# Kernel optimization log

Measured on AMD Instinct MI355X. Metric: run time of the kernel, lower is better.

The kernel has to match this reference:

```python
import jax, jax.numpy as jnp
import numpy as np

N_NODES = 100000
N_QUERIES = 128
D = 128
E = 131072

def leaky(x):
    return jax.nn.leaky_relu(x, negative_slope=0.01)

def setup_inputs() -> dict:
    key = jax.random.key(0)
    ks = jax.random.split(key, 16)
    inp = {
        'visited_node_score': jax.random.uniform(ks[0], (N_NODES,), jnp.float32),
        'node_rep': jax.random.normal(ks[1], (N_NODES, D), jnp.float32),
        'query_src_ts_emb': jax.random.normal(ks[2], (N_QUERIES, D), jnp.float32),
        'query_rel_emb': jax.random.normal(ks[3], (N_QUERIES, D), jnp.float32),
        'rel_emb': jax.random.normal(ks[4], (E, D), jnp.float32),
        'W_left': jax.random.normal(ks[5], (2 * D, 4 * D), jnp.float32) * np.sqrt(2.0 / (4 * D)),
        'b_left': jnp.zeros((2 * D,), jnp.float32),
        'W_right': jax.random.normal(ks[6], (2 * D, 4 * D), jnp.float32) * np.sqrt(2.0 / (4 * D)),
        'b_right': jnp.zeros((2 * D,), jnp.float32),
        'W_center': jax.random.normal(ks[7], (2 * D, 2 * D), jnp.float32) * np.sqrt(2.0 / (4 * D)),
        'b_center': jnp.zeros((2 * D,), jnp.float32),
        'W_step': jax.random.normal(ks[8], (D, D), jnp.float32) * np.sqrt(2.0 / (2 * D)),
        'b_step': jnp.zeros((D,), jnp.float32),
        'query_idx': jax.random.randint(ks[9], (E,), 0, N_QUERIES, jnp.int32),
        'idx_i': jax.random.randint(ks[10], (E,), 0, N_NODES, jnp.int32),
        'idx_j': jax.random.randint(ks[11], (E,), 0, N_NODES, jnp.int32),
        'max_edges': 1024,
    }
    return inp

def _forward(visited_node_score, node_rep, query_src_ts_emb, query_rel_emb, rel_emb,
             W_left, b_left, W_right, b_right, W_center, b_center, W_step, b_step,
             query_idx, idx_i, idx_j, max_edges):
    num_nodes = node_rep.shape[0]
    num_q = query_src_ts_emb.shape[0]
    e = rel_emb.shape[0]
    # gathers (irregular access)
    hi = node_rep[idx_i]            # [E, D]
    hj = node_rep[idx_j]            # [E, D]
    qs = query_src_ts_emb[query_idx]  # [E, D]
    qr = query_rel_emb[query_idx]     # [E, D]
    # G bilinear module: sum(leaky(L x) * C(leaky(R y)), -1)
    left_x = jnp.concatenate([hi, rel_emb, qs, qr], axis=-1)   # [E, 4D]
    right_x = jnp.concatenate([hj, rel_emb, qs, qr], axis=-1)  # [E, 4D]
    l = leaky(left_x @ W_left.T + b_left)                      # [E, 2D]
    r = leaky(right_x @ W_right.T + b_right) @ W_center.T + b_center  # [E, 2D]
    logits = jnp.sum(l * r, axis=-1)                           # [E]
    # segment softmax over source node idx (idx_i), as segment_softmax_op_v2
    seg_max = jax.ops.segment_max(logits, idx_i, num_segments=num_nodes)
    ex = jnp.exp(logits - seg_max[idx_i])
    denom = jax.ops.segment_sum(ex, idx_i, num_segments=num_nodes)
    attn = ex / denom[idx_i]                                   # [E]
    src_score = visited_node_score[idx_i]
    target_score = attn * src_score                            # [E]
    # per-query-group top-k pruning (mask instead of dynamic-shape slice)
    order = jnp.lexsort((-target_score, query_idx))            # sort by group, score desc
    g_sorted = query_idx[order]
    pos = jnp.arange(e, dtype=jnp.int32)
    starts = jax.ops.segment_min(pos, g_sorted, num_segments=num_q)
    rank_sorted = pos - starts[g_sorted]
    rank = jnp.zeros((e,), jnp.int32).at[order].set(rank_sorted)
    keep = (rank < max_edges).astype(logits.dtype)             # [E]
    # sum aggregation of pruned target scores into target nodes (sparse mm)
    updated_node_score = jax.ops.segment_sum(keep * target_score, idx_j, num_segments=num_nodes)
    # update node representation along pruned edges (attention-weighted message passing)
    attn_pruned = keep * attn
    agg = jax.ops.segment_sum(attn_pruned[:, None] * hi, idx_j, num_segments=num_nodes)
    new_rep = node_rep + agg
    # bypass_forward: linear_between_steps + LeakyReLU
    out_rep = leaky(new_rep @ W_step.T + b_step)
    return updated_node_score, out_rep

def reference(visited_node_score, node_rep, query_src_ts_emb, query_rel_emb, rel_emb,
              W_left, b_left, W_right, b_right, W_center, b_center, W_step, b_step,
              query_idx, idx_i, idx_j, max_edges):
    return _forward(visited_node_score, node_rep, query_src_ts_emb, query_rel_emb, rel_emb,
                    W_left, b_left, W_right, b_right, W_center, b_center, W_step, b_step,
                    query_idx, idx_i, idx_j, max_edges)
```

## Files before the change

### kernel.cpp

```cpp
#include <hip/hip_runtime.h>

typedef unsigned short u16;
typedef unsigned int   u32;
typedef __attribute__((ext_vector_type(8))) short short8;
typedef __attribute__((ext_vector_type(4))) short short4v;
typedef __attribute__((ext_vector_type(4))) float f32x4;

#define N_NODES 100000
#define NQ      128
#define DD      128
#define NE      131072
#define OO      256

__device__ __forceinline__ float b2f(u16 b){ u32 u = ((u32)b) << 16; return __uint_as_float(u); }
__device__ __forceinline__ u16 f2b(float f){ u32 u = __float_as_uint(f); u32 r = (u + 0x7FFFu + ((u >> 16) & 1u)) >> 16; return (u16)r; }
__device__ __forceinline__ float lrelu(float x){ return x > 0.0f ? x : 0.01f * x; }
__device__ __forceinline__ u32 fenc(float f){ u32 u = __float_as_uint(f); return (u & 0x80000000u) ? ~u : (u | 0x80000000u); }
__device__ __forceinline__ float fdec(u32 e){ u32 u = (e & 0x80000000u) ? (e & 0x7FFFFFFFu) : ~e; return __uint_as_float(u); }

__device__ __forceinline__ void stage4(f32x4 v, u16* dhi, u16* dlo){
  short4v h4, l4;
  #pragma unroll
  for (int i = 0; i < 4; ++i){
    u16 h = f2b(v[i]); h4[i] = (short)h; l4[i] = (short)f2b(v[i] - b2f(h));
  }
  *(short4v*)dhi = h4; *(short4v*)dlo = l4;
}

__device__ __forceinline__ void cvt4(f32x4 v, short4v& h4, short4v& l4){
  #pragma unroll
  for (int i = 0; i < 4; ++i){
    u16 h = f2b(v[i]); h4[i] = (short)h; l4[i] = (short)f2b(v[i] - b2f(h));
  }
}

#define SPL_N1 (256*512)
#define SPL_N2 (256*512)
#define SPL_N3 (256*256)
#define SPL_N4 (128*128)
__global__ void split_all_kernel(
    const float* __restrict__ Wl, const float* __restrict__ Wr,
    const float* __restrict__ Wc, const float* __restrict__ Ws,
    u16* __restrict__ WlH, u16* __restrict__ WlL,
    u16* __restrict__ WrH, u16* __restrict__ WrL,
    u16* __restrict__ WcH, u16* __restrict__ WcL,
    u16* __restrict__ WsH, u16* __restrict__ WsL)
{
  int i = blockIdx.x*256 + threadIdx.x;
  const float* src; u16 *hi, *lo; int k = i;
  if (k < SPL_N1){ src = Wl; hi = WlH; lo = WlL; }
  else if ((k -= SPL_N1) < SPL_N2){ src = Wr; hi = WrH; lo = WrL; }
  else if ((k -= SPL_N2) < SPL_N3){ src = Wc; hi = WcH; lo = WcL; }
  else if ((k -= SPL_N3) < SPL_N4){ src = Ws; hi = WsH; lo = WsL; }
  else return;
  float x = src[k];
  u16 h = f2b(x);
  hi[k] = h;
  lo[k] = f2b(x - b2f(h));
}

__global__ __launch_bounds__(256) void qtable_kernel(
    const float* __restrict__ qsrc, const float* __restrict__ qrel,
    const float* __restrict__ Wl, const float* __restrict__ bl,
    const float* __restrict__ Wr, const float* __restrict__ br,
    float* __restrict__ Qlt, float* __restrict__ Qrt)
{
  int b = blockIdx.x; int side = b >> 7; int q = b & 127; int o = threadIdx.x;
  __shared__ __align__(16) float s[2*DD];
  __shared__ float sW[256*17];
  if (o < DD) s[o] = qsrc[q*DD + o];
  else        s[o] = qrel[q*DD + o - DD];
  const float* W    = side ? Wr : Wl;
  const float* bias = side ? br : bl;
  float acc = bias[o];
  for (int kt = 0; kt < 16; ++kt){
    __syncthreads();
    for (int f = o; f < 4096; f += 256){
      int oo = f >> 4, kk = f & 15;
      sW[oo*17 + kk] = W[(size_t)oo*512 + 256 + kt*16 + kk];
    }
    __syncthreads();
    #pragma unroll
    for (int kk = 0; kk < 16; ++kk)
      acc += s[kt*16 + kk] * sW[o*17 + kk];
  }
  (side ? Qrt : Qlt)[q*OO + o] = acc;
}

#define BM   64
#define RSTc 264
#define HST  136

template<int WS>
__device__ __forceinline__ void gemm8(f32x4 (&ACC)[4][2],
    const u16* __restrict__ WH, const u16* __restrict__ WL,
    const u16* A0H, const u16* A0L, const u16* A1H, const u16* A1L, int ASTR,
    int ow, int ln, int qd)
{
  short8 pbh[2][2], pbl[2][2];
  #pragma unroll
  for (int d = 0; d < 2; ++d)
    #pragma unroll
    for (int nt = 0; nt < 2; ++nt){ int o = ow + nt*16 + ln;
      pbh[d][nt] = *(const short8*)(WH + (size_t)o*WS + d*32 + qd*8);
      pbl[d][nt] = *(const short8*)(WL + (size_t)o*WS + d*32 + qd*8);
    }
  #pragma unroll
  for (int c = 0; c < 8; ++c){
    const u16* hs = (c < 4) ? A0H : A1H;
    const u16* ls = (c < 4) ? A0L : A1L;
    int cc = (c < 4) ? c : c - 4;
    short8 bh[2], bl[2];
    #pragma unroll
    for (int nt = 0; nt < 2; ++nt){ bh[nt] = pbh[c&1][nt]; bl[nt] = pbl[c&1][nt]; }
    if (c < 6){
      #pragma unroll
      for (int nt = 0; nt < 2; ++nt){ int o = ow + nt*16 + ln;
        pbh[c&1][nt] = *(const short8*)(WH + (size_t)o*WS + (c+2)*32 + qd*8);
        pbl[c&1][nt] = *(const short8*)(WL + (size_t)o*WS + (c+2)*32 + qd*8);
      }
    }
    #pragma unroll
    for (int mp = 0; mp < 2; ++mp){
      short8 ah[2], al[2];
      #pragma unroll
      for (int k = 0; k < 2; ++k){
        int base = ((mp*2 + k)*16 + ln)*ASTR + cc*32 + qd*8;
        ah[k] = *(const short8*)&hs[base];
        al[k] = *(const short8*)&ls[base];
      }
      #pragma unroll
      for (int k = 0; k < 2; ++k)
        #pragma unroll
        for (int nt = 0; nt < 2; ++nt)
          ACC[mp*2+k][nt] = __builtin_amdgcn_mfma_f32_16x16x32_bf16(ah[k], bh[nt], ACC[mp*2+k][nt], 0, 0, 0);
      #pragma unroll
      for (int k = 0; k < 2; ++k)
        #pragma unroll
        for (int nt = 0; nt < 2; ++nt)
          ACC[mp*2+k][nt] = __builtin_amdgcn_mfma_f32_16x16x32_bf16(ah[k], bl[nt], ACC[mp*2+k][nt], 0, 0, 0);
      #pragma unroll
      for (int k = 0; k < 2; ++k)
        #pragma unroll
        for (int nt = 0; nt < 2; ++nt)
          ACC[mp*2+k][nt] = __builtin_amdgcn_mfma_f32_16x16x32_bf16(al[k], bh[nt], ACC[mp*2+k][nt], 0, 0, 0);
    }
  }
}

__global__ __launch_bounds__(512, 4) void edge_logits_kernel(
    const float* __restrict__ node_rep, const float* __restrict__ rel_emb,
    const u16* __restrict__ WlH, const u16* __restrict__ WlL,
    const u16* __restrict__ WrH, const u16* __restrict__ WrL,
    const u16* __restrict__ WcH, const u16* __restrict__ WcL,
    const float* __restrict__ bcb,
    const float* __restrict__ Qlt, const float* __restrict__ Qrt,
    const int* __restrict__ idx_i, const int* __restrict__ idx_j, const int* __restrict__ qidx,
    float* __restrict__ logits, u32* __restrict__ segmax, int* __restrict__ qcount)
{
  __shared__ __align__(16) u16 bufA[2*BM*HST];
  __shared__ __align__(16) u16 bufB[2*BM*HST];
  __shared__ int qidS[BM];
  __shared__ float lpart[8][BM];

  u16* HjHi = bufA;  u16* HjLo = bufA + BM*HST;
  u16* ReHi = bufB;  u16* ReLo = bufB + BM*HST;
  u16* RRhi = bufA;  u16* RRlo = bufB;

  const int tid = threadIdx.x;
  const int e0 = blockIdx.x * BM;
  const int lane = tid & 63, w = tid >> 6;
  const int ln = lane & 15, qd = lane >> 4;
  const int ow = w * 32;

  if (tid < BM) qidS[tid] = qidx[e0 + tid];

  #pragma unroll
  for (int it = 0; it < 4; ++it){
    int c = tid + it*512;
    int r = c >> 5, seg = (c & 31) << 2;
    int j = idx_j[e0 + r];
    f32x4 vj = *(const f32x4*)(node_rep + (size_t)j*DD + seg);
    f32x4 vr = *(const f32x4*)(rel_emb + (size_t)(e0 + r)*DD + seg);
    stage4(vj, &HjHi[r*HST + seg], &HjLo[r*HST + seg]);
    stage4(vr, &ReHi[r*HST + seg], &ReLo[r*HST + seg]);
  }
  short4v hpreH[4], hpreL[4];
  #pragma unroll
  for (int it = 0; it < 4; ++it){
    int c = tid + it*512;
    int r = c >> 5, seg = (c & 31) << 2;
    f32x4 v = *(const f32x4*)(node_rep + (size_t)idx_i[e0 + r]*DD + seg);
    cvt4(v, hpreH[it], hpreL[it]);
  }
  __syncthreads();

  f32x4 acc[4][2];
  #pragma unroll
  for (int mt = 0; mt < 4; ++mt)
    #pragma unroll
    for (int nt = 0; nt < 2; ++nt) acc[mt][nt] = (f32x4){0.f,0.f,0.f,0.f};
  gemm8<512>(acc, WrH, WrL, HjHi, HjLo, ReHi, ReLo, HST, ow, ln, qd);
  __syncthreads();

  #pragma unroll
  for (int it = 0; it < 4; ++it){
    int c = tid + it*512;
    int r = c >> 5, seg = (c & 31) << 2;
    *(short4v*)&HjHi[r*HST + seg] = hpreH[it];
    *(short4v*)&HjLo[r*HST + seg] = hpreL[it];
  }
  __syncthreads();

  f32x4 lacc[4][2];
  #pragma unroll
  for (int mt = 0; mt < 4; ++mt)
    #pragma unroll
    for (int nt = 0; nt < 2; ++nt) lacc[mt][nt] = (f32x4){0.f,0.f,0.f,0.f};
  gemm8<512>(lacc, WlH, WlL, HjHi, HjLo, ReHi, ReLo, HST, ow, ln, qd);
  __syncthreads();

  #pragma unroll
  for (int mt = 0; mt < 4; ++mt)
    #pragma unroll
    for (int nt = 0; nt < 2; ++nt){
      int col = ow + nt*16 + ln;
      #pragma unroll
      for (int rg = 0; rg < 4; ++rg){
        int row = mt*16 + qd*4 + rg;
        float v = acc[mt][nt][rg] + Qrt[qidS[row]*OO + col];
        v = lrelu(v);
        u16 hi = f2b(v);
        RRhi[row*RSTc + col] = hi;
        RRlo[row*RSTc + col] = f2b(v - b2f(hi));
      }
    }
  __syncthreads();

  f32x4 racc[4][2];
  #pragma unroll
  for (int mt = 0; mt < 4; ++mt)
    #pragma unroll
    for (int nt = 0; nt < 2; ++nt) racc[mt][nt] = (f32x4){0.f,0.f,0.f,0.f};
  gemm8<256>(racc, WcH, WcL, RRhi, RRlo, RRhi + 128, RRlo + 128, RSTc, ow, ln, qd);

  float bcv[2];
  #pragma unroll
  for (int nt = 0; nt < 2; ++nt) bcv[nt] = bcb[ow + nt*16 + ln];

  float part[4][4];
  #pragma unroll
  for (int mt = 0; mt < 4; ++mt)
    #pragma unroll
    for (int rg = 0; rg < 4; ++rg) part[mt][rg] = 0.f;

  #pragma unroll
  for (int mt = 0; mt < 4; ++mt)
    #pragma unroll
    for (int nt = 0; nt < 2; ++nt){
      int col = ow + nt*16 + ln;
      #pragma unroll
      for (int rg = 0; rg < 4; ++rg){
        int row = mt*16 + qd*4 + rg;
        float lv = lacc[mt][nt][rg] + Qlt[qidS[row]*OO + col];
        lv = lrelu(lv);
        float rv = racc[mt][nt][rg] + bcv[nt];
        part[mt][rg] += lv * rv;
      }
    }

  #pragma unroll
  for (int mt = 0; mt < 4; ++mt)
    #pragma unroll
    for (int rg = 0; rg < 4; ++rg){
      float p = part[mt][rg];
      p += __shfl_xor(p, 1); p += __shfl_xor(p, 2);
      p += __shfl_xor(p, 4); p += __shfl_xor(p, 8);
      if (ln == 0) lpart[w][mt*16 + qd*4 + rg] = p;
    }
  __syncthreads();
  if (tid < BM){
    float lg = lpart[0][tid] + lpart[1][tid] + lpart[2][tid] + lpart[3][tid]
             + lpart[4][tid] + lpart[5][tid] + lpart[6][tid] + lpart[7][tid];
    int e = e0 + tid;
    logits[e] = lg;
    atomicMax(segmax + idx_i[e], fenc(lg));
    atomicAdd(qcount + qidx[e], 1);
  }
}

__global__ void seg_exp_sum_kernel(const float* __restrict__ logits,
    const int* __restrict__ idx_i, const u32* __restrict__ segmax,
    float* __restrict__ ex, float* __restrict__ denom)
{
  int e = blockIdx.x*256 + threadIdx.x; if (e >= NE) return;
  int i = idx_i[e];
  float d = fminf(logits[e] - fdec(segmax[i]), 0.0f);
  float v = expf(d);
  ex[e] = v;
  atomicAdd(denom + i, v);
}

__global__ __launch_bounds__(128) void scan_kernel(const int* __restrict__ qcount,
                            int* __restrict__ qstart, int* __restrict__ qcursor)
{
  __shared__ int s[NQ];
  int t = threadIdx.x;
  int mine = qcount[t];
  s[t] = mine;
  __syncthreads();
  #pragma unroll
  for (int off = 1; off < NQ; off <<= 1){
    int v = (t >= off) ? s[t - off] : 0;
    __syncthreads();
    s[t] += v;
    __syncthreads();
  }
  int excl = s[t] - mine;
  qstart[t] = excl;
  qcursor[t] = excl;
}

__global__ void attn_bucket_kernel(const float* __restrict__ ex,
    const float* __restrict__ denom, const int* __restrict__ idx_i,
    const float* __restrict__ visited, const int* __restrict__ qidx,
    int* __restrict__ qcursor, int* __restrict__ bucket,
    float* __restrict__ attn, float* __restrict__ target)
{
  int e = blockIdx.x*256 + threadIdx.x; if (e >= NE) return;
  int i = idx_i[e];
  float a = ex[e] / fmaxf(denom[i], 1e-30f);
  attn[e] = a;
  target[e] = a * visited[i];
  int p = atomicAdd(qcursor + qidx[e], 1);
  bucket[p] = e;
}

#define TOPK_CAP 2560
__global__ __launch_bounds__(1024) void topk_kernel(
    const int* __restrict__ qcount, const int* __restrict__ qstart,
    const int* __restrict__ bucket, const float* __restrict__ target,
    const int* __restrict__ maxe_p, int* __restrict__ keep)
{
  __shared__ float ss[TOPK_CAP];
  __shared__ int   se[TOPK_CAP];
  int q = blockIdx.x;
  int m = qcount[q], start = qstart[q];
  int maxe = *maxe_p;
  if (maxe <= 0 || maxe > (1 << 30)){
    float f = __int_as_float(maxe);
    if (f > 0.0f && f < 1.0e9f) maxe = (int)f;
  }
  int tid = threadIdx.x;
  if (m <= maxe){
    for (int i = tid; i < m; i += 1024) keep[bucket[start + i]] = 1;
    return;
  }
  if (m <= TOPK_CAP){
    for (int i = tid; i < m; i += 1024){
      int e = bucket[start + i]; ss[i] = target[e]; se[i] = e;
    }
    __syncthreads();
    for (int i = tid; i < m; i += 1024){
      float s = ss[i]; int eid = se[i]; int cnt = 0;
      for (int j = 0; j < m; ++j){
        float sj = ss[j]; int ej = se[j];
        cnt += (sj > s) || (sj == s && ej < eid);
      }
      keep[eid] = (cnt < maxe) ? 1 : 0;
    }
  } else {
    for (int i = tid; i < m; i += 1024){
      int eid = bucket[start + i]; float s = target[eid]; int cnt = 0;
      for (int j = 0; j < m; ++j){
        int ej = bucket[start + j]; float sj = target[ej];
        cnt += (sj > s) || (sj == s && ej < eid);
      }
      keep[eid] = (cnt < maxe) ? 1 : 0;
    }
  }
}

__global__ __launch_bounds__(256) void edge_scatter_kernel(
    const int* __restrict__ keep, const float* __restrict__ attn,
    const float* __restrict__ target,
    const int* __restrict__ idx_i, const int* __restrict__ idx_j,
    const float* __restrict__ node_rep,
    float* __restrict__ out_score, float* __restrict__ agg)
{
  int wid = (blockIdx.x * 256 + threadIdx.x) >> 6;
  if (wid >= NE) return;
  if (!keep[wid]) return;
  int lane = threadIdx.x & 63;
  int ii = idx_i[wid], jj = idx_j[wid];
  float a = attn[wid];
  if (lane == 0) atomicAdd(out_score + jj, target[wid]);
  float h0 = node_rep[(size_t)ii*DD + lane];
  float h1 = node_rep[(size_t)ii*DD + 64 + lane];
  atomicAdd(agg + (size_t)jj*DD + lane,      a*h0);
  atomicAdd(agg + (size_t)jj*DD + 64 + lane, a*h1);
}

__global__ __launch_bounds__(256) void final_mfma_kernel(
    const float* __restrict__ node_rep, const float* __restrict__ aggc,
    const u16* __restrict__ WsH, const u16* __restrict__ WsL,
    const float* __restrict__ bstep, float* __restrict__ out_rep)
{
  __shared__ __align__(16) u16 Ahi[64*HST];
  __shared__ __align__(16) u16 Alo[64*HST];
  const int tid = threadIdx.x;
  const int m0 = blockIdx.x * 64;

  for (int c = tid; c < 64*32; c += 256){
    int r = c >> 5, seg = (c & 31) << 2;
    int m = m0 + r;
    float v[4];
    if (m < N_NODES){
      const float* nr = node_rep + (size_t)m*DD + seg;
      const float* ag = aggc + (size_t)m*DD + seg;
      #pragma unroll
      for (int i = 0; i < 4; ++i) v[i] = nr[i] + ag[i];
    } else {
      #pragma unroll
      for (int i = 0; i < 4; ++i) v[i] = 0.f;
    }
    short4v h4, l4;
    #pragma unroll
    for (int i = 0; i < 4; ++i){
      u16 h = f2b(v[i]); h4[i] = (short)h; l4[i] = (short)f2b(v[i] - b2f(h));
    }
    *(short4v*)&Ahi[r*HST + seg] = h4;
    *(short4v*)&Alo[r*HST + seg] = l4;
  }
  __syncthreads();

  const int lane = tid & 63, w = tid >> 6;
  const int ln = lane & 15, qd = lane >> 4;
  const int ow = w * 32;

  short8 bh[2][4], bl[2][4];
  #pragma unroll
  for (int nt = 0; nt < 2; ++nt)
    #pragma unroll
    for (int c = 0; c < 4; ++c){
      int o = ow + nt*16 + ln;
      bh[nt][c] = *(const short8*)(WsH + (size_t)o*DD + c*32 + qd*8);
      bl[nt][c] = *(const short8*)(WsL + (size_t)o*DD + c*32 + qd*8);
    }

  f32x4 acc[4][2];
  #pragma unroll
  for (int mt = 0; mt < 4; ++mt)
    #pragma unroll
    for (int nt = 0; nt < 2; ++nt) acc[mt][nt] = (f32x4){0.f,0.f,0.f,0.f};

  #pragma unroll
  for (int mt = 0; mt < 4; ++mt)
    #pragma unroll
    for (int c = 0; c < 4; ++c){
      int base = (mt*16 + ln)*HST + c*32 + qd*8;
      short8 ah = *(const short8*)&Ahi[base];
      short8 al = *(const short8*)&Alo[base];
      #pragma unroll
      for (int nt = 0; nt < 2; ++nt){
        acc[mt][nt] = __builtin_amdgcn_mfma_f32_16x16x32_bf16(ah, bh[nt][c], acc[mt][nt], 0, 0, 0);
        acc[mt][nt] = __builtin_amdgcn_mfma_f32_16x16x32_bf16(ah, bl[nt][c], acc[mt][nt], 0, 0, 0);
        acc[mt][nt] = __builtin_amdgcn_mfma_f32_16x16x32_bf16(al, bh[nt][c], acc[mt][nt], 0, 0, 0);
      }
    }

  #pragma unroll
  for (int mt = 0; mt < 4; ++mt)
    #pragma unroll
    for (int nt = 0; nt < 2; ++nt){
      int col = ow + nt*16 + ln;
      float bs = bstep[col];
      #pragma unroll
      for (int rg = 0; rg < 4; ++rg){
        int m = m0 + mt*16 + qd*4 + rg;
        if (m < N_NODES)
          out_rep[(size_t)m*DD + col] = lrelu(acc[mt][nt][rg] + bs);
      }
    }
}

extern "C" void kernel_launch(void* const* d_in, const int* in_sizes, int n_in,
                              void* d_out, int out_size, void* d_ws, size_t ws_size,
                              hipStream_t stream)
{
  const float* visited  = (const float*)d_in[0];
  const float* node_rep = (const float*)d_in[1];
  const float* qsrc     = (const float*)d_in[2];
  const float* qrel     = (const float*)d_in[3];
  const float* rel_emb  = (const float*)d_in[4];
  const float* Wl       = (const float*)d_in[5];
  const float* bl       = (const float*)d_in[6];
  const float* Wr       = (const float*)d_in[7];
  const float* br       = (const float*)d_in[8];
  const float* Wc       = (const float*)d_in[9];
  const float* bcb      = (const float*)d_in[10];
  const float* Wstep    = (const float*)d_in[11];
  const float* bstep    = (const float*)d_in[12];
  const int* qidx       = (const int*)d_in[13];
  const int* idx_i      = (const int*)d_in[14];
  const int* idx_j      = (const int*)d_in[15];
  const int* maxe       = (const int*)d_in[16];

  char* wp = (char*)d_ws;
  size_t used = 0;
  auto alloc = [&](size_t bytes)->char*{
    size_t pad = (bytes + 255) & ~(size_t)255;
    char* p = wp + used; used += pad; return p;
  };
  float* Qlt    = (float*)alloc((size_t)NQ*OO*4);
  float* Qrt    = (float*)alloc((size_t)NQ*OO*4);
  float* logits = (float*)alloc((size_t)NE*4);
  float* ex     = (float*)alloc((size_t)NE*4);
  float* attn   = (float*)alloc((size_t)NE*4);
  float* target = (float*)alloc((size_t)NE*4);
  u32*   segmax = (u32*)  alloc((size_t)N_NODES*4);
  float* denom  = (float*)alloc((size_t)N_NODES*4);
  int*   qcount = (int*)  alloc((size_t)NQ*4);
  int*   qstart = (int*)  alloc((size_t)NQ*4);
  int*   qcursor= (int*)  alloc((size_t)NQ*4);
  int*   bucket = (int*)  alloc((size_t)NE*4);
  int*   keep   = (int*)  alloc((size_t)NE*4);
  u16* WlH = (u16*)alloc((size_t)256*512*2); u16* WlL = (u16*)alloc((size_t)256*512*2);
  u16* WrH = (u16*)alloc((size_t)256*512*2); u16* WrL = (u16*)alloc((size_t)256*512*2);
  u16* WcH = (u16*)alloc((size_t)256*256*2); u16* WcL = (u16*)alloc((size_t)256*256*2);
  u16* WsH = (u16*)alloc((size_t)128*128*2); u16* WsL = (u16*)alloc((size_t)128*128*2);
  (void)ws_size; (void)in_sizes; (void)n_in; (void)out_size;

  float* out_score = (float*)d_out;
  float* out_rep   = (float*)d_out + N_NODES;

  hipMemsetAsync(d_out, 0, ((size_t)N_NODES + (size_t)N_NODES*DD)*4, stream);
  hipMemsetAsync(segmax, 0, (size_t)N_NODES*4, stream);
  hipMemsetAsync(denom,  0, (size_t)N_NODES*4, stream);
  hipMemsetAsync(qcount, 0, (size_t)NQ*4,      stream);
  hipMemsetAsync(keep,   0, (size_t)NE*4,      stream);

  {
    int n_all = SPL_N1 + SPL_N2 + SPL_N3 + SPL_N4;
    split_all_kernel<<<(n_all + 255)/256, 256, 0, stream>>>(Wl, Wr, Wc, Wstep,
        WlH, WlL, WrH, WrL, WcH, WcL, WsH, WsL);
  }

  qtable_kernel<<<256, 256, 0, stream>>>(qsrc, qrel, Wl, bl, Wr, br, Qlt, Qrt);

  edge_logits_kernel<<<NE/BM, 512, 0, stream>>>(node_rep, rel_emb,
      WlH, WlL, WrH, WrL, WcH, WcL, bcb, Qlt, Qrt, idx_i, idx_j, qidx,
      logits, segmax, qcount);

  seg_exp_sum_kernel<<<NE/256, 256, 0, stream>>>(logits, idx_i, segmax, ex, denom);
  scan_kernel<<<1, 128, 0, stream>>>(qcount, qstart, qcursor);
  attn_bucket_kernel<<<NE/256, 256, 0, stream>>>(ex, denom, idx_i, visited, qidx,
                                                 qcursor, bucket, attn, target);
  topk_kernel<<<NQ, 1024, 0, stream>>>(qcount, qstart, bucket, target, maxe, keep);

  edge_scatter_kernel<<<NE/4, 256, 0, stream>>>(keep, attn, target, idx_i, idx_j,
                                                node_rep, out_score, out_rep);
  final_mfma_kernel<<<(N_NODES + 63)/64, 256, 0, stream>>>(node_rep, out_rep,
                                               WsH, WsL, bstep, out_rep);
}
```

Measured before the change: 849.3 us.

## Fuse edge scatter into final matmul via destination-sorted CSR buckets

Builds a CSR grouping of edges by destination node (count, three-stage scan, bucket fill) and fuses the attention-weighted aggregation into the final MFMA kernel. Each block accumulates its 64 destination rows in shared memory using LDS atomics instead of global atomics. This removes the large output memset and the round trip of agg through global memory. The cost is extra scan kernels and global atomics in the bucketing step, plus per-element bf16 splitting moved into the inner MFMA loop.

```diff
diff --git a/kernel.cpp b/kernel.cpp
--- a/kernel.cpp
+++ b/kernel.cpp
@@ -11,6 +11,7 @@
 #define DD      128
 #define NE      131072
 #define OO      256
+#define NCH     391
 
 __device__ __forceinline__ float b2f(u16 b){ u32 u = ((u32)b) << 16; return __uint_as_float(u); }
 __device__ __forceinline__ u16 f2b(float f){ u32 u = __float_as_uint(f); u32 r = (u + 0x7FFFu + ((u >> 16) & 1u)) >> 16; return (u16)r; }
@@ -290,8 +291,9 @@
 }
 
 __global__ void seg_exp_sum_kernel(const float* __restrict__ logits,
-    const int* __restrict__ idx_i, const u32* __restrict__ segmax,
-    float* __restrict__ ex, float* __restrict__ denom)
+    const int* __restrict__ idx_i, const int* __restrict__ idx_j,
+    const u32* __restrict__ segmax,
+    float* __restrict__ ex, float* __restrict__ denom, int* __restrict__ jcount)
 {
   int e = blockIdx.x*256 + threadIdx.x; if (e >= NE) return;
   int i = idx_i[e];
@@ -299,6 +301,7 @@
   float v = expf(d);
   ex[e] = v;
   atomicAdd(denom + i, v);
+  atomicAdd(jcount + idx_j[e], 1);
 }
 
 __global__ __launch_bounds__(128) void scan_kernel(const int* __restrict__ qcount,
@@ -321,10 +324,71 @@
   qcursor[t] = excl;
 }
 
+__global__ __launch_bounds__(256) void jscan_a(const int* __restrict__ jcount,
+                                               int* __restrict__ csum)
+{
+  __shared__ int s[256];
+  int b = blockIdx.x, t = threadIdx.x;
+  int i = b*256 + t;
+  s[t] = (i < N_NODES) ? jcount[i] : 0;
+  __syncthreads();
+  #pragma unroll
+  for (int off = 128; off > 0; off >>= 1){
+    if (t < off) s[t] += s[t + off];
+    __syncthreads();
+  }
+  if (t == 0) csum[b] = s[0];
+}
+
+__global__ __launch_bounds__(512) void jscan_b(const int* __restrict__ csum,
+                                               int* __restrict__ coff,
+                                               int* __restrict__ jstart)
+{
+  __shared__ int s[512];
+  int t = threadIdx.x;
+  int v = (t < NCH) ? csum[t] : 0;
+  s[t] = v;
+  __syncthreads();
+  #pragma unroll
+  for (int off = 1; off < 512; off <<= 1){
+    int u = (t >= off) ? s[t - off] : 0;
+    __syncthreads();
+    s[t] += u;
+    __syncthreads();
+  }
+  if (t < NCH) coff[t] = s[t] - v;
+  if (t == 0) jstart[N_NODES] = NE;
+}
+
+__global__ __launch_bounds__(256) void jscan_c(const int* __restrict__ jcount,
+    const int* __restrict__ coff, int* __restrict__ jstart, int* __restrict__ jcursor)
+{
+  __shared__ int s[256];
+  int b = blockIdx.x, t = threadIdx.x;
+  int i = b*256 + t;
+  int mine = (i < N_NODES) ? jcount[i] : 0;
+  s[t] = mine;
+  __syncthreads();
+  #pragma unroll
+  for (int off = 1; off < 256; off <<= 1){
+    int u = (t >= off) ? s[t - off] : 0;
+    __syncthreads();
+    s[t] += u;
+    __syncthreads();
+  }
+  if (i < N_NODES){
+    int excl = coff[b] + s[t] - mine;
+    jstart[i] = excl;
+    jcursor[i] = excl;
+  }
+}
+
 __global__ void attn_bucket_kernel(const float* __restrict__ ex,
     const float* __restrict__ denom, const int* __restrict__ idx_i,
+    const int* __restrict__ idx_j,
     const float* __restrict__ visited, const int* __restrict__ qidx,
     int* __restrict__ qcursor, int* __restrict__ bucket,
+    int* __restrict__ jcursor, int* __restrict__ jbucket,
     float* __restrict__ attn, float* __restrict__ target)
 {
   int e = blockIdx.x*256 + threadIdx.x; if (e >= NE) return;
@@ -334,6 +398,8 @@
   target[e] = a * visited[i];
   int p = atomicAdd(qcursor + qidx[e], 1);
   bucket[p] = e;
+  int p2 = atomicAdd(jcursor + idx_j[e], 1);
+  jbucket[p2] = e;
 }
 
 #define TOPK_CAP 2560
@@ -381,62 +447,53 @@
   }
 }
 
-__global__ __launch_bounds__(256) void edge_scatter_kernel(
+#define PADF 132
+__global__ __launch_bounds__(256) void final_fused_kernel(
+    const float* __restrict__ node_rep,
+    const int* __restrict__ jstart, const int* __restrict__ jbucket,
     const int* __restrict__ keep, const float* __restrict__ attn,
     const float* __restrict__ target,
     const int* __restrict__ idx_i, const int* __restrict__ idx_j,
-    const float* __restrict__ node_rep,
-    float* __restrict__ out_score, float* __restrict__ agg)
-{
-  int wid = (blockIdx.x * 256 + threadIdx.x) >> 6;
-  if (wid >= NE) return;
-  if (!keep[wid]) return;
-  int lane = threadIdx.x & 63;
-  int ii = idx_i[wid], jj = idx_j[wid];
-  float a = attn[wid];
-  if (lane == 0) atomicAdd(out_score + jj, target[wid]);
-  float h0 = node_rep[(size_t)ii*DD + lane];
-  float h1 = node_rep[(size_t)ii*DD + 64 + lane];
-  atomicAdd(agg + (size_t)jj*DD + lane,      a*h0);
-  atomicAdd(agg + (size_t)jj*DD + 64 + lane, a*h1);
-}
-
-__global__ __launch_bounds__(256) void final_mfma_kernel(
-    const float* __restrict__ node_rep, const float* __restrict__ aggc,
     const u16* __restrict__ WsH, const u16* __restrict__ WsL,
-    const float* __restrict__ bstep, float* __restrict__ out_rep)
-{
-  __shared__ __align__(16) u16 Ahi[64*HST];
-  __shared__ __align__(16) u16 Alo[64*HST];
+    const float* __restrict__ bstep,
+    float* __restrict__ out_score, float* __restrict__ out_rep)
+{
+  __shared__ __align__(16) float Af[64*PADF];
+  __shared__ float scoreS[64];
   const int tid = threadIdx.x;
   const int m0 = blockIdx.x * 64;
+  const int lane = tid & 63, wv = tid >> 6;
 
   for (int c = tid; c < 64*32; c += 256){
     int r = c >> 5, seg = (c & 31) << 2;
     int m = m0 + r;
-    float v[4];
-    if (m < N_NODES){
-      const float* nr = node_rep + (size_t)m*DD + seg;
-      const float* ag = aggc + (size_t)m*DD + seg;
-      #pragma unroll
-      for (int i = 0; i < 4; ++i) v[i] = nr[i] + ag[i];
-    } else {
-      #pragma unroll
-      for (int i = 0; i < 4; ++i) v[i] = 0.f;
-    }
-    short4v h4, l4;
-    #pragma unroll
-    for (int i = 0; i < 4; ++i){
-      u16 h = f2b(v[i]); h4[i] = (short)h; l4[i] = (short)f2b(v[i] - b2f(h));
-    }
-    *(short4v*)&Ahi[r*HST + seg] = h4;
-    *(short4v*)&Alo[r*HST + seg] = l4;
-  }
-  __syncthreads();
-
-  const int lane = tid & 63, w = tid >> 6;
+    f32x4 v = (m < N_NODES) ? *(const f32x4*)(node_rep + (size_t)m*DD + seg)
+                            : (f32x4){0.f,0.f,0.f,0.f};
+    *(f32x4*)&Af[r*PADF + seg] = v;
+  }
+  if (tid < 64) scoreS[tid] = 0.f;
+  __syncthreads();
+
+  int lo = jstart[m0];
+  int hi = jstart[(m0 + 64 < N_NODES) ? (m0 + 64) : N_NODES];
+  for (int p = lo + wv; p < hi; p += 4){
+    int e = jbucket[p];
+    if (!keep[e]) continue;
+    int ii = idx_i[e];
+    float a = attn[e];
+    int row = idx_j[e] - m0;
+    float h0 = node_rep[(size_t)ii*DD + lane];
+    float h1 = node_rep[(size_t)ii*DD + 64 + lane];
+    atomicAdd(&Af[row*PADF + lane],      a*h0);
+    atomicAdd(&Af[row*PADF + 64 + lane], a*h1);
+    if (lane == 0) atomicAdd(&scoreS[row], target[e]);
+  }
+  __syncthreads();
+
+  if (tid < 64 && m0 + tid < N_NODES) out_score[m0 + tid] = scoreS[tid];
+
   const int ln = lane & 15, qd = lane >> 4;
-  const int ow = w * 32;
+  const int ow = wv * 32;
 
   short8 bh[2][4], bl[2][4];
   #pragma unroll
@@ -458,9 +515,18 @@
   for (int mt = 0; mt < 4; ++mt)
     #pragma unroll
     for (int c = 0; c < 4; ++c){
-      int base = (mt*16 + ln)*HST + c*32 + qd*8;
-      short8 ah = *(const short8*)&Ahi[base];
-      short8 al = *(const short8*)&Alo[base];
+      const float* ap = &Af[(mt*16 + ln)*PADF + c*32 + qd*8];
+      f32x4 a0 = *(const f32x4*)ap;
+      f32x4 a1 = *(const f32x4*)(ap + 4);
+      short8 ah, al;
+      #pragma unroll
+      for (int i = 0; i < 4; ++i){
+        u16 h = f2b(a0[i]); ah[i] = (short)h; al[i] = (short)f2b(a0[i] - b2f(h));
+      }
+      #pragma unroll
+      for (int i = 0; i < 4; ++i){
+        u16 h = f2b(a1[i]); ah[4+i] = (short)h; al[4+i] = (short)f2b(a1[i] - b2f(h));
+      }
       #pragma unroll
       for (int nt = 0; nt < 2; ++nt){
         acc[mt][nt] = __builtin_amdgcn_mfma_f32_16x16x32_bf16(ah, bh[nt][c], acc[mt][nt], 0, 0, 0);
@@ -525,6 +591,12 @@
   int*   qcursor= (int*)  alloc((size_t)NQ*4);
   int*   bucket = (int*)  alloc((size_t)NE*4);
   int*   keep   = (int*)  alloc((size_t)NE*4);
+  int*   jcount = (int*)  alloc((size_t)N_NODES*4);
+  int*   jstart = (int*)  alloc(((size_t)N_NODES + 1)*4);
+  int*   jcursor= (int*)  alloc((size_t)N_NODES*4);
+  int*   jbucket= (int*)  alloc((size_t)NE*4);
+  int*   csum   = (int*)  alloc((size_t)NCH*4);
+  int*   coff   = (int*)  alloc((size_t)NCH*4);
   u16* WlH = (u16*)alloc((size_t)256*512*2); u16* WlL = (u16*)alloc((size_t)256*512*2);
   u16* WrH = (u16*)alloc((size_t)256*512*2); u16* WrL = (u16*)alloc((size_t)256*512*2);
   u16* WcH = (u16*)alloc((size_t)256*256*2); u16* WcL = (u16*)alloc((size_t)256*256*2);
@@ -534,9 +606,9 @@
   float* out_score = (float*)d_out;
   float* out_rep   = (float*)d_out + N_NODES;
 
-  hipMemsetAsync(d_out, 0, ((size_t)N_NODES + (size_t)N_NODES*DD)*4, stream);
   hipMemsetAsync(segmax, 0, (size_t)N_NODES*4, stream);
   hipMemsetAsync(denom,  0, (size_t)N_NODES*4, stream);
+  hipMemsetAsync(jcount, 0, (size_t)N_NODES*4, stream);
   hipMemsetAsync(qcount, 0, (size_t)NQ*4,      stream);
   hipMemsetAsync(keep,   0, (size_t)NE*4,      stream);
 
@@ -552,14 +624,19 @@
       WlH, WlL, WrH, WrL, WcH, WcL, bcb, Qlt, Qrt, idx_i, idx_j, qidx,
       logits, segmax, qcount);
 
-  seg_exp_sum_kernel<<<NE/256, 256, 0, stream>>>(logits, idx_i, segmax, ex, denom);
+  seg_exp_sum_kernel<<<NE/256, 256, 0, stream>>>(logits, idx_i, idx_j, segmax,
+                                                 ex, denom, jcount);
   scan_kernel<<<1, 128, 0, stream>>>(qcount, qstart, qcursor);
-  attn_bucket_kernel<<<NE/256, 256, 0, stream>>>(ex, denom, idx_i, visited, qidx,
-                                                 qcursor, bucket, attn, target);
+  jscan_a<<<NCH, 256, 0, stream>>>(jcount, csum);
+  jscan_b<<<1, 512, 0, stream>>>(csum, coff, jstart);
+  jscan_c<<<NCH, 256, 0, stream>>>(jcount, coff, jstart, jcursor);
+
+  attn_bucket_kernel<<<NE/256, 256, 0, stream>>>(ex, denom, idx_i, idx_j,
+                                                 visited, qidx, qcursor, bucket,
+                                                 jcursor, jbucket, attn, target);
   topk_kernel<<<NQ, 1024, 0, stream>>>(qcount, qstart, bucket, target, maxe, keep);
 
-  edge_scatter_kernel<<<NE/4, 256, 0, stream>>>(keep, attn, target, idx_i, idx_j,
-                                                node_rep, out_score, out_rep);
-  final_mfma_kernel<<<(N_NODES + 63)/64, 256, 0, stream>>>(node_rep, out_rep,
-                                               WsH, WsL, bstep, out_rep);
-}
+  final_fused_kernel<<<(N_NODES + 63)/64, 256, 0, stream>>>(node_rep,
+      jstart, jbucket, keep, attn, target, idx_i, idx_j,
+      WsH, WsL, bstep, out_score, out_rep);
+}
```

Result: slower. 888.2 us (+4.6%).
